# Kernel tuning notes

Hardware: AMD Instinct MI355X
Metric: run time of the kernel (lower is better)

## Reference

```python
import jax, jax.numpy as jnp
import numpy as np

B, E, H, N_TAYLOR = 8192, 256, 4096, 4
BN_EPS = 1e-5


def setup_inputs() -> dict:
    key = jax.random.key(0)
    ks = jax.random.split(key, 6)
    s = 0.02
    return {
        "z1": jax.random.normal(ks[0], (B, E), jnp.float32),
        "z2": jax.random.normal(ks[1], (B, E), jnp.float32),
        "p1": jax.random.normal(ks[2], (B, E), jnp.float32),
        "p2": jax.random.normal(ks[3], (B, E), jnp.float32),
        "W1": jax.random.normal(ks[4], (E, H), jnp.float32) * s,
        "gamma": jnp.ones((H,), jnp.float32),
        "beta": jnp.zeros((H,), jnp.float32),
        "W2": jax.random.normal(ks[5], (H, E), jnp.float32) * s,
        "b2": jnp.zeros((E,), jnp.float32),
        "lamda_inv": jnp.asarray(100.0, jnp.float32),
    }


def _predictor(z, W1, gamma, beta, W2, b2):
    h = z @ W1                                   # [B, H]
    mu = jnp.mean(h, axis=0)
    var = jnp.mean(jnp.square(h - mu), axis=0)   # biased var (torch BN training)
    h = (h - mu) * jax.lax.rsqrt(var + BN_EPS) * gamma + beta
    h = jax.nn.relu(h)
    return h @ W2 + b2                           # [B, E]


def _l2norm(x):
    n = jnp.linalg.norm(x, axis=1, keepdims=True)
    return x / jnp.maximum(n, 1e-12)


def _mec(view1, view2, lamda_inv):
    v1, v2 = _l2norm(view1), _l2norm(view2)
    c = (v1 @ v2.T) / lamda_inv                  # [B, B]
    power = c
    sum_p = jnp.zeros_like(c)
    for k in range(1, N_TAYLOR + 1):
        if k > 1:
            power = power @ c
        sign = 1.0 if (k + 1) % 2 == 0 else -1.0
        sum_p = sum_p + sign * power / k
    return jnp.trace(sum_p)


def reference(z1, z2, p1, p2, W1, gamma, beta, W2, b2, lamda_inv):
    q1 = _predictor(z1, W1, gamma, beta, W2, b2)
    q2 = _predictor(z2, W1, gamma, beta, W2, b2)
    loss = (_mec(p1, q2, lamda_inv) + _mec(p2, q1, lamda_inv)) * 0.5 / B
    return -loss * lamda_inv
```

## Files before the change

### kernel.cpp

```cpp
#include <hip/hip_runtime.h>

#define B_ROWS 8192
#define E_DIM  256
#define H_DIM  4096

typedef __attribute__((ext_vector_type(8))) short short8;
typedef __attribute__((ext_vector_type(4))) float f32x4;

typedef __attribute__((address_space(1))) const void* gas1_t;
typedef __attribute__((address_space(3))) void*       las3_t;

__device__ __forceinline__ float b2f(unsigned short s) {
    return __uint_as_float(((unsigned)s) << 16);
}
__device__ __forceinline__ unsigned short f2b(float f) {
    unsigned u = __float_as_uint(f);
    u += 0x7fffu + ((u >> 16) & 1u);
    return (unsigned short)(u >> 16);
}

__device__ __forceinline__ unsigned cvt_pk_bf16(float lo, float hi) {
    unsigned r;
    asm("v_cvt_pk_bf16_f32 %0, %1, %2" : "=v"(r) : "v"(lo), "v"(hi));
    return r;
}

__device__ __forceinline__ void lds_barrier() {
    asm volatile("s_waitcnt lgkmcnt(0)\n\ts_barrier" ::: "memory");
}

__device__ __forceinline__ int swz(int row, int slot) {
    return slot ^ ((row >> 1) & 3);
}

__global__ void k_transpose_cast2(const float* __restrict__ W1,
                                  unsigned short* __restrict__ W1T,
                                  const float* __restrict__ W2,
                                  unsigned short* __restrict__ W2T) {
    const int bid = blockIdx.x;
    const int m = bid >> 10, b = bid & 1023;
    const float* in; unsigned short* out; int R, C, cx, cy;
    if (m == 0) { in = W1; out = W1T; R = E_DIM; C = H_DIM; cx = b & 127; cy = b >> 7; }
    else        { in = W2; out = W2T; R = H_DIM; C = E_DIM; cx = b & 7;   cy = b >> 3; }
    const int c0 = cx * 32, r0 = cy * 32;

    __shared__ float tile[32][33];
    const int tx = threadIdx.x & 31, ty = threadIdx.x >> 5;
#pragma unroll
    for (int j = 0; j < 4; ++j)
        tile[ty * 4 + j][tx] = in[(size_t)(r0 + ty * 4 + j) * C + c0 + tx];
    __syncthreads();
#pragma unroll
    for (int j = 0; j < 4; ++j)
        out[(size_t)(c0 + ty * 4 + j) * R + r0 + tx] = f2b(tile[tx][ty * 4 + j]);
}

__global__ void k_cast2(const float* __restrict__ z1, unsigned short* __restrict__ o1,
                        const float* __restrict__ z2, unsigned short* __restrict__ o2) {
    const float* in = blockIdx.y ? z2 : z1;
    unsigned short* out = blockIdx.y ? o2 : o1;
    int i = blockIdx.x * blockDim.x + threadIdx.x;
    float4 v = ((const float4*)in)[i];
    ushort4 o;
    o.x = f2b(v.x); o.y = f2b(v.y); o.z = f2b(v.z); o.w = f2b(v.w);
    ((ushort4*)out)[i] = o;
}

__global__ __launch_bounds__(256) void k_gemm1(
    const unsigned short* __restrict__ A, const unsigned short* __restrict__ Bt,
    unsigned short* __restrict__ Cout,
    float* __restrict__ cs, float* __restrict__ cs2,
    int M, int N, int K) {
    constexpr int BK = 32, BM = 128, BN = 128;
    constexpr int MI = 4, NI = 4;
    __shared__ __align__(16) short As[BM * BK];
    __shared__ __align__(16) short Bs[BN * BK];

    const int t = threadIdx.x;
    const int lane = t & 63, wv = t >> 6;
    const int wr = wv >> 1, wc = wv & 1;
    const int l15 = lane & 15, quad = lane >> 4;
    const int m0 = blockIdx.y * BM, n0 = blockIdx.x * BN;

    f32x4 acc[MI][NI] = {};

    for (int k0 = 0; k0 < K; k0 += BK) {
#pragma unroll
        for (int q = 0; q < 2; ++q) {
            int u = q * 256 + t;
            int row = u >> 2, kc = swz(row, u & 3);
            const short* gp = (const short*)A + (size_t)(m0 + row) * K + k0 + kc * 8;
            short* lp = As + (size_t)(q * 256 + (wv << 6)) * 8;
            __builtin_amdgcn_global_load_lds((gas1_t)gp, (las3_t)lp, 16, 0, 0);
        }
#pragma unroll
        for (int q = 0; q < 2; ++q) {
            int u = q * 256 + t;
            int row = u >> 2, kc = swz(row, u & 3);
            const short* gp = (const short*)Bt + (size_t)(n0 + row) * K + k0 + kc * 8;
            short* lp = Bs + (size_t)(q * 256 + (wv << 6)) * 8;
            __builtin_amdgcn_global_load_lds((gas1_t)gp, (las3_t)lp, 16, 0, 0);
        }
        __syncthreads();

        short8 af[MI], bfr[NI];
#pragma unroll
        for (int mi = 0; mi < MI; ++mi) {
            int row = wr * 64 + mi * 16 + l15;
            af[mi] = *(const short8*)(As + row * BK + (swz(row, quad) << 3));
        }
#pragma unroll
        for (int ni = 0; ni < NI; ++ni) {
            int row = wc * 64 + ni * 16 + l15;
            bfr[ni] = *(const short8*)(Bs + row * BK + (swz(row, quad) << 3));
        }
#pragma unroll
        for (int mi = 0; mi < MI; ++mi)
#pragma unroll
            for (int ni = 0; ni < NI; ++ni)
                acc[mi][ni] = __builtin_amdgcn_mfma_f32_16x16x32_bf16(
                    af[mi], bfr[ni], acc[mi][ni], 0, 0, 0);
        __syncthreads();
    }

#pragma unroll
    for (int ni = 0; ni < NI; ++ni) {
        float s = 0.f, s2 = 0.f;
#pragma unroll
        for (int mi = 0; mi < MI; ++mi)
#pragma unroll
            for (int r = 0; r < 4; ++r) {
                int row = m0 + wr * 64 + mi * 16 + quad * 4 + r;
                int col = n0 + wc * 64 + ni * 16 + l15;
                float v = acc[mi][ni][r];
                Cout[(size_t)row * N + col] = f2b(v);
                s += v; s2 += v * v;
            }
        s  += __shfl_xor(s, 16);  s  += __shfl_xor(s, 32);
        s2 += __shfl_xor(s2, 16); s2 += __shfl_xor(s2, 32);
        if (quad == 0) {
            int col = n0 + wc * 64 + ni * 16 + l15;
            atomicAdd(&cs[col], s);
            atomicAdd(&cs2[col], s2);
        }
    }
}

__global__ void k_bnprep(const float* __restrict__ sum, const float* __restrict__ sumsq,
                         const float* __restrict__ gamma, const float* __restrict__ beta,
                         unsigned* __restrict__ ssb) {
    int j = blockIdx.x * 256 + threadIdx.x;
    float mu = sum[j] * (1.f / B_ROWS);
    float var = sumsq[j] * (1.f / B_ROWS) - mu * mu;
    float sc = gamma[j] * rsqrtf(var + 1e-5f);
    float sh = beta[j] - mu * sc;
    ssb[j] = ((unsigned)f2b(sc) << 16) | (unsigned)f2b(sh);
}

__device__ __forceinline__ short8 bnrelu8(uint4 hv, uint4 sa, uint4 sb) {
    const unsigned short* hu = (const unsigned short*)&hv;
    const unsigned* wa = (const unsigned*)&sa;
    const unsigned* wb = (const unsigned*)&sb;
    float f[8];
#pragma unroll
    for (int j = 0; j < 8; ++j) {
        unsigned w = j < 4 ? wa[j] : wb[j - 4];
        float sc = __uint_as_float(w & 0xffff0000u);
        float sh = __uint_as_float(w << 16);
        f[j] = fmaxf(b2f(hu[j]) * sc + sh, 0.f);
    }
    union { unsigned u[4]; short8 s; } o;
#pragma unroll
    for (int j = 0; j < 4; ++j) o.u[j] = cvt_pk_bf16(f[2 * j], f[2 * j + 1]);
    return o.s;
}

__global__ __launch_bounds__(256, 4) void k_gemm2d(
    const unsigned short* __restrict__ A, const unsigned short* __restrict__ Bt,
    float* __restrict__ Cout, const float* __restrict__ bias,
    const unsigned* __restrict__ ssb,
    int M, int N, int K) {
    constexpr int BK = 64, BM = 32, BN = 128;
    constexpr int NI = 4;
    __shared__ __align__(16) short As[2][BM * BK];
    __shared__ __align__(16) short Bs[2][BN * BK];

    const int t = threadIdx.x;
    const int lane = t & 63, wv = t >> 6;
    const int wr = wv >> 1, wc = wv & 1;
    const int l15 = lane & 15, quad = lane >> 4;

    const int bid = blockIdx.x;
    const int xcd = bid & 7, sl = bid >> 3;
    const int xp = sl & 1, pidx = (sl >> 1) * 8 + xcd;
    const int m0 = (pidx & 255) * BM;
    const int n0 = xp * BN;
    const int bz = pidx >> 8;

    const int Kc = K >> 1;
    const int kbeg = bz * Kc;
    const int ITERS = Kc / BK;

    const int arow = t >> 3, aks = t & 7;
    const unsigned short* hp = A + (size_t)(m0 + arow) * K + aks * 8;
    const unsigned* ssp = ssb + aks * 8;
    const int aswz = (aks ^ (arow & 7)) << 3;
    const int awoff = arow * BK + aswz;

    const unsigned short* bp0 = Bt + (size_t)(n0 + arow) * K + aks * 8;
    const int bwoff0 = arow * BK + aswz;

    f32x4 acc[NI] = {};

    uint4 hreg = *(const uint4*)(hp + kbeg);
    uint4 sa = *(const uint4*)(ssp + kbeg);
    uint4 sb = *(const uint4*)(ssp + kbeg + 4);
    uint4 b0 = *(const uint4*)(bp0 + kbeg);
    uint4 b1 = *(const uint4*)(bp0 + (size_t)32 * K + kbeg);
    uint4 b2r = *(const uint4*)(bp0 + (size_t)64 * K + kbeg);
    uint4 b3 = *(const uint4*)(bp0 + (size_t)96 * K + kbeg);

    for (int i = 0; i < ITERS; ++i) {
        const int k0 = kbeg + i * BK;
        short* Ab = As[i & 1];
        short* Bb = Bs[i & 1];

        *(short8*)(Ab + awoff) = bnrelu8(hreg, sa, sb);
        *(uint4*)(Bb + bwoff0)           = b0;
        *(uint4*)(Bb + bwoff0 + 32 * BK) = b1;
        *(uint4*)(Bb + bwoff0 + 64 * BK) = b2r;
        *(uint4*)(Bb + bwoff0 + 96 * BK) = b3;
        lds_barrier();

        const int kn = (i + 1 < ITERS) ? k0 + BK : kbeg;
        hreg = *(const uint4*)(hp + kn);
        sa = *(const uint4*)(ssp + kn);
        sb = *(const uint4*)(ssp + kn + 4);
        b0 = *(const uint4*)(bp0 + kn);
        b1 = *(const uint4*)(bp0 + (size_t)32 * K + kn);
        b2r = *(const uint4*)(bp0 + (size_t)64 * K + kn);
        b3 = *(const uint4*)(bp0 + (size_t)96 * K + kn);

        short8 af[2], bfr[2][NI];
        {
            int row = wr * 16 + l15;
            af[0] = *(const short8*)(Ab + row * BK + (((quad)     ^ (row & 7)) << 3));
            af[1] = *(const short8*)(Ab + row * BK + (((4 + quad) ^ (row & 7)) << 3));
        }
#pragma unroll
        for (int ni = 0; ni < NI; ++ni) {
            int row = wc * 64 + ni * 16 + l15;
            bfr[0][ni] = *(const short8*)(Bb + row * BK + (((quad)     ^ (row & 7)) << 3));
            bfr[1][ni] = *(const short8*)(Bb + row * BK + (((4 + quad) ^ (row & 7)) << 3));
        }
#pragma unroll
        for (int kk = 0; kk < 2; ++kk)
#pragma unroll
            for (int ni = 0; ni < NI; ++ni)
                acc[ni] = __builtin_amdgcn_mfma_f32_16x16x32_bf16(
                    af[kk], bfr[kk][ni], acc[ni], 0, 0, 0);
    }

#pragma unroll
    for (int ni = 0; ni < NI; ++ni)
#pragma unroll
        for (int r = 0; r < 4; ++r) {
            int row = m0 + wr * 16 + quad * 4 + r;
            int col = n0 + wc * 64 + ni * 16 + l15;
            float v = acc[ni][r];
            if (bz == 0) v += bias[col];
            atomicAdd(&Cout[(size_t)row * N + col], v);
        }
}

__global__ __launch_bounds__(256) void k_ntc(
    const float* __restrict__ x0, const float* __restrict__ x1,
    const float* __restrict__ x2, const float* __restrict__ x3,
    unsigned short* __restrict__ o0, unsigned short* __restrict__ o1,
    unsigned short* __restrict__ o2, unsigned short* __restrict__ o3) {
    const int z = blockIdx.y;
    const float* x = z == 0 ? x0 : z == 1 ? x1 : z == 2 ? x2 : x3;
    unsigned short* out = z == 0 ? o0 : z == 1 ? o1 : z == 2 ? o2 : o3;

    __shared__ float tile[32][264];
    __shared__ float red[32][8];
    __shared__ float invs[32];
    const int t = threadIdx.x;
    const int r0 = blockIdx.x * 32;

#pragma unroll
    for (int i = 0; i < 8; ++i) {
        int u = i * 256 + t;
        int row = u >> 6, cp = (u & 63) * 4;
        float4 v = *(const float4*)(x + (size_t)(r0 + row) * E_DIM + cp);
        *(float4*)&tile[row][cp] = v;
    }
    __syncthreads();
    {
        int row = t >> 3, cg = (t & 7) * 32;
        float s = 0.f;
#pragma unroll
        for (int j = 0; j < 32; ++j) { float v = tile[row][cg + j]; s += v * v; }
        red[row][t & 7] = s;
    }
    __syncthreads();
    if (t < 32) {
        float s = 0.f;
#pragma unroll
        for (int j = 0; j < 8; ++j) s += red[t][j];
        invs[t] = 1.f / fmaxf(sqrtf(s), 1e-12f);
    }
    __syncthreads();
    {
        int row = t & 31, cb = (t >> 5) * 32;
        float inv = invs[row];
#pragma unroll
        for (int j = 0; j < 32; ++j) {
            int c = cb + j;
            out[(size_t)c * B_ROWS + r0 + row] = f2b(tile[row][c] * inv);
        }
    }
}

#define GKS 16
__global__ __launch_bounds__(256) void k_gram(
    const unsigned short* __restrict__ p1T, const unsigned short* __restrict__ q2T,
    const unsigned short* __restrict__ p2T, const unsigned short* __restrict__ q1T,
    float* __restrict__ Ma, float* __restrict__ Mb) {
    constexpr int BK = 32;
    const int mec = blockIdx.z >> 4, kz = blockIdx.z & 15;
    const unsigned short* A = mec ? p2T : p1T;
    const unsigned short* Bt = mec ? q1T : q2T;
    float* Mout = mec ? Mb : Ma;

    __shared__ __align__(16) short As[64 * BK];
    __shared__ __align__(16) short Bs[64 * BK];

    const int t = threadIdx.x;
    const int lane = t & 63, wv = t >> 6;
    const int wr = wv >> 1, wc = wv & 1;
    const int l15 = lane & 15, quad = lane >> 4;
    const int m0 = blockIdx.y * 64, n0 = blockIdx.x * 64;
    const int kbeg = kz * (B_ROWS / GKS);

    f32x4 acc[2][2] = {};

    for (int k0 = kbeg; k0 < kbeg + B_ROWS / GKS; k0 += BK) {
        {
            int row = t >> 2, kc = swz(row, t & 3);
            const short* gpa = (const short*)A + (size_t)(m0 + row) * B_ROWS + k0 + kc * 8;
            short* lpa = As + (size_t)(wv << 6) * 8;
            __builtin_amdgcn_global_load_lds((gas1_t)gpa, (las3_t)lpa, 16, 0, 0);
            const short* gpb = (const short*)Bt + (size_t)(n0 + row) * B_ROWS + k0 + kc * 8;
            short* lpb = Bs + (size_t)(wv << 6) * 8;
            __builtin_amdgcn_global_load_lds((gas1_t)gpb, (las3_t)lpb, 16, 0, 0);
        }
        __syncthreads();

        short8 af[2], bfr[2];
#pragma unroll
        for (int mi = 0; mi < 2; ++mi) {
            int row = wr * 32 + mi * 16 + l15;
            af[mi] = *(const short8*)(As + row * BK + (swz(row, quad) << 3));
        }
#pragma unroll
        for (int ni = 0; ni < 2; ++ni) {
            int row = wc * 32 + ni * 16 + l15;
            bfr[ni] = *(const short8*)(Bs + row * BK + (swz(row, quad) << 3));
        }
#pragma unroll
        for (int mi = 0; mi < 2; ++mi)
#pragma unroll
            for (int ni = 0; ni < 2; ++ni)
                acc[mi][ni] = __builtin_amdgcn_mfma_f32_16x16x32_bf16(
                    af[mi], bfr[ni], acc[mi][ni], 0, 0, 0);
        __syncthreads();
    }

#pragma unroll
    for (int mi = 0; mi < 2; ++mi)
#pragma unroll
        for (int ni = 0; ni < 2; ++ni)
#pragma unroll
            for (int r = 0; r < 4; ++r) {
                int row = m0 + wr * 32 + mi * 16 + quad * 4 + r;
                int col = n0 + wc * 32 + ni * 16 + l15;
                atomicAdd(&Mout[(size_t)row * E_DIM + col], acc[mi][ni][r]);
            }
}

__global__ void k_m2(const float* __restrict__ Ma, const float* __restrict__ Mb,
                     float* __restrict__ M2a, float* __restrict__ M2b) {
    const float* M = blockIdx.z ? Mb : Ma;
    float* M2 = blockIdx.z ? M2b : M2a;
    int b = blockIdx.x * 16 + (threadIdx.x & 15);
    int a = blockIdx.y * 16 + (threadIdx.x >> 4);
    float s = 0.f;
    for (int k = 0; k < E_DIM; ++k) s += M[a * E_DIM + k] * M[k * E_DIM + b];
    M2[a * E_DIM + b] = s;
}

__global__ __launch_bounds__(256) void k_traces2(
    const float* __restrict__ Ma, const float* __restrict__ M2a,
    const float* __restrict__ Mb, const float* __restrict__ M2b,
    const float* __restrict__ lam, float* __restrict__ out) {
    const float* M  = blockIdx.z ? Mb  : Ma;
    const float* M2 = blockIdx.z ? M2b : M2a;
    const int i0 = blockIdx.y * 32, j0 = blockIdx.x * 32;
    const int t = threadIdx.x, col = t & 31, row = t >> 5;

    __shared__ float A[32][33], Bt[32][33], A2[32][33], B2[32][33];
#pragma unroll
    for (int r = 0; r < 4; ++r) {
        int rr = r * 8 + row;
        A [rr][col] = M [(i0 + rr) * E_DIM + j0 + col];
        Bt[rr][col] = M [(j0 + rr) * E_DIM + i0 + col];
        A2[rr][col] = M2[(i0 + rr) * E_DIM + j0 + col];
        B2[rr][col] = M2[(j0 + rr) * E_DIM + i0 + col];
    }
    __syncthreads();

    float lamv = lam[0];
    float il = 1.f / lamv;
    float F = -0.5f * lamv * (1.f / B_ROWS);
    float c1 = F * il;
    float c2 = -F * 0.5f * il * il;
    float c3 = F * (1.f / 3.f) * il * il * il;
    float c4 = -F * 0.25f * il * il * il * il;

    float s = 0.f;
#pragma unroll
    for (int r = 0; r < 4; ++r) {
        int rr = r * 8 + row;
        float mij = A[rr][col], mji = Bt[col][rr];
        float m2ij = A2[rr][col], m2ji = B2[col][rr];
        s += c2 * mij * mji + c3 * m2ij * mji + c4 * m2ij * m2ji;
        if (i0 + rr == j0 + col) s += c1 * mij;
    }
#pragma unroll
    for (int o = 32; o; o >>= 1) s += __shfl_down(s, o);
    __shared__ float red[4];
    if ((t & 63) == 0) red[t >> 6] = s;
    __syncthreads();
    if (t == 0) atomicAdd(out, red[0] + red[1] + red[2] + red[3]);
}

extern "C" void kernel_launch(void* const* d_in, const int* in_sizes, int n_in,
                              void* d_out, int out_size, void* d_ws, size_t ws_size,
                              hipStream_t stream) {
    const float* z1 = (const float*)d_in[0];
    const float* z2 = (const float*)d_in[1];
    const float* p1 = (const float*)d_in[2];
    const float* p2 = (const float*)d_in[3];
    const float* W1 = (const float*)d_in[4];
    const float* gamma = (const float*)d_in[5];
    const float* beta = (const float*)d_in[6];
    const float* W2 = (const float*)d_in[7];
    const float* b2 = (const float*)d_in[8];
    const float* lam = (const float*)d_in[9];
    float* out = (float*)d_out;
    char* ws = (char*)d_ws;

    size_t off = 0;
    auto alloc = [&](size_t bytes) { size_t o = off; off += (bytes + 255) & ~(size_t)255; return o; };
    unsigned short* W1T = (unsigned short*)(ws + alloc((size_t)E_DIM * H_DIM * 2));
    unsigned short* W2T = (unsigned short*)(ws + alloc((size_t)H_DIM * E_DIM * 2));
    unsigned short* zb1 = (unsigned short*)(ws + alloc((size_t)B_ROWS * E_DIM * 2));
    unsigned short* zb2 = (unsigned short*)(ws + alloc((size_t)B_ROWS * E_DIM * 2));
    unsigned short* h   = (unsigned short*)(ws + alloc((size_t)B_ROWS * H_DIM * 2));
    float* q1 = (float*)(ws + alloc((size_t)B_ROWS * E_DIM * 4));
    float* q2 = (float*)(ws + alloc((size_t)B_ROWS * E_DIM * 4));
    float* Ma  = (float*)(ws + alloc((size_t)E_DIM * E_DIM * 4));
    float* Mb  = (float*)(ws + alloc((size_t)E_DIM * E_DIM * 4));
    float* M2a = (float*)(ws + alloc((size_t)E_DIM * E_DIM * 4));
    float* M2b = (float*)(ws + alloc((size_t)E_DIM * E_DIM * 4));
    float* cs0 = (float*)(ws + alloc(H_DIM * 4));
    float* cs0q = (float*)(ws + alloc(H_DIM * 4));
    float* cs1 = (float*)(ws + alloc(H_DIM * 4));
    float* cs1q = (float*)(ws + alloc(H_DIM * 4));
    unsigned* ssb = (unsigned*)(ws + alloc(H_DIM * 4));

    const size_t TSZ = (size_t)E_DIM * B_ROWS;
    unsigned short* p1T = h;
    unsigned short* q2T = h + TSZ;
    unsigned short* p2T = h + 2 * TSZ;
    unsigned short* q1T = h + 3 * TSZ;

    hipMemsetAsync(out, 0, sizeof(float), stream);
    hipMemsetAsync(q1, 0, ((size_t)2 * B_ROWS * E_DIM + 2 * E_DIM * E_DIM) * 4, stream);
    hipMemsetAsync(cs0, 0, (size_t)4 * H_DIM * 4, stream);

    k_transpose_cast2<<<dim3(2048), 256, 0, stream>>>(W1, W1T, W2, W2T);
    k_cast2<<<dim3(B_ROWS * E_DIM / 4 / 256, 2), 256, 0, stream>>>(z1, zb1, z2, zb2);

    const unsigned short* zbs[2] = {zb1, zb2};
    float* qs[2] = {q1, q2};
    float* css[2] = {cs0, cs1};
    float* cssq[2] = {cs0q, cs1q};
    for (int v = 0; v < 2; ++v) {
        k_gemm1<<<dim3(H_DIM / 128, B_ROWS / 128), 256, 0, stream>>>(
            zbs[v], W1T, h, css[v], cssq[v], B_ROWS, H_DIM, E_DIM);
        k_bnprep<<<dim3(H_DIM / 256), 256, 0, stream>>>(css[v], cssq[v], gamma, beta, ssb);
        k_gemm2d<<<dim3(1024), 256, 0, stream>>>(
            h, W2T, qs[v], b2, ssb, B_ROWS, E_DIM, H_DIM);
    }

    k_ntc<<<dim3(B_ROWS / 32, 4), 256, 0, stream>>>(
        p1, q2, p2, q1, p1T, q2T, p2T, q1T);

    k_gram<<<dim3(4, 4, 2 * GKS), 256, 0, stream>>>(p1T, q2T, p2T, q1T, Ma, Mb);
    k_m2<<<dim3(16, 16, 2), 256, 0, stream>>>(Ma, Mb, M2a, M2b);
    k_traces2<<<dim3(8, 8, 2), 256, 0, stream>>>(Ma, M2a, Mb, M2b, lam, out);
}
```

Measured before the change: 302.7 us.

## Double-buffer gemm1 LDS tiles with register-prefetched global loads

Replaces the direct global-to-LDS loads in the first GEMM with loads into registers, issued one k-step ahead. Each tile is then written to one of two alternating LDS buffers, so global memory latency can overlap with the MFMA work on the current tile. It doubles LDS usage and adds register pressure. The loop keeps two barriers per iteration, which limits how much overlap it gains. The lds_barrier helper is assumed to be defined in the hidden part of the file.

```diff
diff --git a/kernel.cpp b/kernel.cpp
--- a/kernel.cpp
+++ b/kernel.cpp
@@ -73,8 +73,8 @@
     int M, int N, int K) {
     constexpr int BK = 32, BM = 128, BN = 128;
     constexpr int MI = 4, NI = 4;
-    __shared__ __align__(16) short As[BM * BK];
-    __shared__ __align__(16) short Bs[BN * BK];
+    __shared__ __align__(16) short As[2][BM * BK];
+    __shared__ __align__(16) short Bs[2][BN * BK];
 
     const int t = threadIdx.x;
     const int lane = t & 63, wv = t >> 6;
@@ -82,37 +82,49 @@
     const int l15 = lane & 15, quad = lane >> 4;
     const int m0 = blockIdx.y * BM, n0 = blockIdx.x * BN;
 
+    const int ITERS = K / BK;
+
+    const int r0s = t >> 2, sl = t & 3;
+    const unsigned short* ap0 = A + (size_t)(m0 + r0s) * K + sl * 8;
+    const unsigned short* ap1 = A + (size_t)(m0 + 64 + r0s) * K + sl * 8;
+    const unsigned short* bp0 = Bt + (size_t)(n0 + r0s) * K + sl * 8;
+    const unsigned short* bp1 = Bt + (size_t)(n0 + 64 + r0s) * K + sl * 8;
+    const int awo0 = r0s * BK + (swz(r0s, sl) << 3);
+    const int awo1 = (64 + r0s) * BK + (swz(64 + r0s, sl) << 3);
+
     f32x4 acc[MI][NI] = {};
 
-    for (int k0 = 0; k0 < K; k0 += BK) {
-#pragma unroll
-        for (int q = 0; q < 2; ++q) {
-            int u = q * 256 + t;
-            int row = u >> 2, kc = swz(row, u & 3);
-            const short* gp = (const short*)A + (size_t)(m0 + row) * K + k0 + kc * 8;
-            short* lp = As + (size_t)(q * 256 + (wv << 6)) * 8;
-            __builtin_amdgcn_global_load_lds((gas1_t)gp, (las3_t)lp, 16, 0, 0);
-        }
-#pragma unroll
-        for (int q = 0; q < 2; ++q) {
-            int u = q * 256 + t;
-            int row = u >> 2, kc = swz(row, u & 3);
-            const short* gp = (const short*)Bt + (size_t)(n0 + row) * K + k0 + kc * 8;
-            short* lp = Bs + (size_t)(q * 256 + (wv << 6)) * 8;
-            __builtin_amdgcn_global_load_lds((gas1_t)gp, (las3_t)lp, 16, 0, 0);
-        }
-        __syncthreads();
+    uint4 a0 = *(const uint4*)(ap0);
+    uint4 a1 = *(const uint4*)(ap1);
+    uint4 b0 = *(const uint4*)(bp0);
+    uint4 b1 = *(const uint4*)(bp1);
+
+    for (int i = 0; i < ITERS; ++i) {
+        short* Ab = As[i & 1];
+        short* Bb = Bs[i & 1];
+
+        *(uint4*)(Ab + awo0) = a0;
+        *(uint4*)(Ab + awo1) = a1;
+        *(uint4*)(Bb + awo0) = b0;
+        *(uint4*)(Bb + awo1) = b1;
+        lds_barrier();
+
+        const int kn = (i + 1 < ITERS) ? (i + 1) * BK : 0;
+        a0 = *(const uint4*)(ap0 + kn);
+        a1 = *(const uint4*)(ap1 + kn);
+        b0 = *(const uint4*)(bp0 + kn);
+        b1 = *(const uint4*)(bp1 + kn);
 
         short8 af[MI], bfr[NI];
 #pragma unroll
         for (int mi = 0; mi < MI; ++mi) {
             int row = wr * 64 + mi * 16 + l15;
-            af[mi] = *(const short8*)(As + row * BK + (swz(row, quad) << 3));
+            af[mi] = *(const short8*)(Ab + row * BK + (swz(row, quad) << 3));
         }
 #pragma unroll
         for (int ni = 0; ni < NI; ++ni) {
             int row = wc * 64 + ni * 16 + l15;
-            bfr[ni] = *(const short8*)(Bs + row * BK + (swz(row, quad) << 3));
+            bfr[ni] = *(const short8*)(Bb + row * BK + (swz(row, quad) << 3));
         }
 #pragma unroll
         for (int mi = 0; mi < MI; ++mi)
@@ -120,7 +132,7 @@
             for (int ni = 0; ni < NI; ++ni)
                 acc[mi][ni] = __builtin_amdgcn_mfma_f32_16x16x32_bf16(
                     af[mi], bfr[ni], acc[mi][ni], 0, 0, 0);
-        __syncthreads();
+        lds_barrier();
     }
 
 #pragma unroll
```

Measured after the change: 305.1 us. No clear change (+0.8%).

## Double-buffer LDS in gram kernel with register prefetch of next K tile

Applied to the files above, without the earlier changes.

Replaces the direct global-to-LDS loads and the two barriers per K step in the gram kernel with register-staged prefetch and double-buffered shared memory. The next tile's global loads are issued before the current tile's MFMAs, so memory latency can overlap compute, and one barrier per iteration is removed. It adds register pressure and doubles the LDS footprint. A dummy reload on the last iteration wastes a small amount of bandwidth.

```diff
diff --git a/kernel.cpp b/kernel.cpp
--- a/kernel.cpp
+++ b/kernel.cpp
@@ -333,8 +333,8 @@
     const unsigned short* Bt = mec ? q1T : q2T;
     float* Mout = mec ? Mb : Ma;
 
-    __shared__ __align__(16) short As[64 * BK];
-    __shared__ __align__(16) short Bs[64 * BK];
+    __shared__ __align__(16) short As[2][64 * BK];
+    __shared__ __align__(16) short Bs[2][64 * BK];
 
     const int t = threadIdx.x;
     const int lane = t & 63, wv = t >> 6;
@@ -342,31 +342,40 @@
     const int l15 = lane & 15, quad = lane >> 4;
     const int m0 = blockIdx.y * 64, n0 = blockIdx.x * 64;
     const int kbeg = kz * (B_ROWS / GKS);
+    const int ITERS = (B_ROWS / GKS) / BK;
+
+    const int r0s = t >> 2, sl = t & 3;
+    const unsigned short* ap = A + (size_t)(m0 + r0s) * B_ROWS + sl * 8;
+    const unsigned short* bp = Bt + (size_t)(n0 + r0s) * B_ROWS + sl * 8;
+    const int awo = r0s * BK + (swz(r0s, sl) << 3);
 
     f32x4 acc[2][2] = {};
 
-    for (int k0 = kbeg; k0 < kbeg + B_ROWS / GKS; k0 += BK) {
-        {
-            int row = t >> 2, kc = swz(row, t & 3);
-            const short* gpa = (const short*)A + (size_t)(m0 + row) * B_ROWS + k0 + kc * 8;
-            short* lpa = As + (size_t)(wv << 6) * 8;
-            __builtin_amdgcn_global_load_lds((gas1_t)gpa, (las3_t)lpa, 16, 0, 0);
-            const short* gpb = (const short*)Bt + (size_t)(n0 + row) * B_ROWS + k0 + kc * 8;
-            short* lpb = Bs + (size_t)(wv << 6) * 8;
-            __builtin_amdgcn_global_load_lds((gas1_t)gpb, (las3_t)lpb, 16, 0, 0);
-        }
-        __syncthreads();
+    uint4 a0 = *(const uint4*)(ap + kbeg);
+    uint4 b0 = *(const uint4*)(bp + kbeg);
+
+    for (int i = 0; i < ITERS; ++i) {
+        short* Ab = As[i & 1];
+        short* Bb = Bs[i & 1];
+
+        *(uint4*)(Ab + awo) = a0;
+        *(uint4*)(Bb + awo) = b0;
+        lds_barrier();
+
+        const int kn = kbeg + ((i + 1 < ITERS) ? (i + 1) * BK : 0);
+        a0 = *(const uint4*)(ap + kn);
+        b0 = *(const uint4*)(bp + kn);
 
         short8 af[2], bfr[2];
 #pragma unroll
         for (int mi = 0; mi < 2; ++mi) {
             int row = wr * 32 + mi * 16 + l15;
-            af[mi] = *(const short8*)(As + row * BK + (swz(row, quad) << 3));
+            af[mi] = *(const short8*)(Ab + row * BK + (swz(row, quad) << 3));
         }
 #pragma unroll
         for (int ni = 0; ni < 2; ++ni) {
             int row = wc * 32 + ni * 16 + l15;
-            bfr[ni] = *(const short8*)(Bs + row * BK + (swz(row, quad) << 3));
+            bfr[ni] = *(const short8*)(Bb + row * BK + (swz(row, quad) << 3));
         }
 #pragma unroll
         for (int mi = 0; mi < 2; ++mi)
@@ -374,7 +383,6 @@
             for (int ni = 0; ni < 2; ++ni)
                 acc[mi][ni] = __builtin_amdgcn_mfma_f32_16x16x32_bf16(
                     af[mi], bfr[ni], acc[mi][ni], 0, 0, 0);
-        __syncthreads();
     }
 
 #pragma unroll
```

New measurement: 301.7 us. Within noise of the previous version (-0.3%).
